# Optimization experiments

Measured on AMD Instinct MI355X. Metric: run time of the kernel, lower is better.

The kernel has to match this reference:

```python
import jax, jax.numpy as jnp
import numpy as np

N_NODES = 100000
N_EDGES = 3200000
NFEAT, H1, H2, NCLASS = 512, 300, 200, 40


def setup_inputs() -> dict:
    key = jax.random.key(0)
    ks = jax.random.split(key, 8)
    x = jax.random.normal(ks[0], (N_NODES, NFEAT), dtype=jnp.float32)
    edge_index = jax.random.randint(ks[1], (2, N_EDGES), 0, N_NODES, dtype=jnp.int32)
    edge_weight = jax.random.uniform(ks[2], (N_EDGES,), dtype=jnp.float32)
    def glorot(k, fi, fo):
        s = 1.0 / np.sqrt(fi)
        return jax.random.uniform(k, (fi, fo), jnp.float32, -s, s)
    w1 = glorot(ks[3], NFEAT, H1)
    w2 = glorot(ks[4], H1, H2)
    w3 = glorot(ks[5], H2, NCLASS)
    return {
        'x': x, 'edge_index': edge_index, 'edge_weight': edge_weight,
        'w1': w1, 'b1': jnp.zeros((H1,), jnp.float32),
        'w2': w2, 'b2': jnp.zeros((H2,), jnp.float32),
        'w3': w3, 'b3': jnp.zeros((NCLASS,), jnp.float32),
    }


def _gcn_layer(h, edge_index, edge_weight, w, b):
    # support = h @ W ; out = A @ support + b  (A given as weighted edge list)
    support = h @ w                                   # [N, out]
    src, dst = edge_index[0], edge_index[1]
    msgs = support[src] * edge_weight[:, None]        # gather + scale, [E, out]
    agg = jax.ops.segment_sum(msgs, dst, num_segments=h.shape[0])
    return agg + b


def reference(x, edge_index, edge_weight, w1, b1, w2, b2, w3, b3):
    h1 = jax.nn.relu(_gcn_layer(x, edge_index, edge_weight, w1, b1))
    h2 = jax.nn.relu(_gcn_layer(h1, edge_index, edge_weight, w2, b2))
    logits = _gcn_layer(h2, edge_index, edge_weight, w3, b3)
    return jax.nn.softmax(logits, axis=1)
```

## Files before the change

kernel.cpp:

```cpp
#include <hip/hip_runtime.h>
#include <hip/hip_bf16.h>
#include <hip/hip_fp16.h>
#include <math.h>

#define NFEAT 512
#define H1 300
#define H2 200
#define NCLASS 40

typedef __attribute__((ext_vector_type(8))) _Float16 half8;
typedef __attribute__((ext_vector_type(4))) float f32x4;
typedef __attribute__((ext_vector_type(2))) unsigned int u32x2;

__device__ __forceinline__ void stage16(const void* gptr, void* ldsptr) {
    __builtin_amdgcn_global_load_lds(
        (const __attribute__((address_space(1))) unsigned int*)gptr,
        (__attribute__((address_space(3))) unsigned int*)ldsptr,
        16, 0, 0);
}

__device__ __forceinline__ unsigned short f2h(float f) {
    return __half_as_ushort(__float2half(f));
}
__device__ __forceinline__ float h2f(unsigned short u) {
    return __half2float(__ushort_as_half(u));
}
__device__ __forceinline__ float2 h2f2(unsigned int u) {
    __half2 h = *reinterpret_cast<__half2*>(&u);
    return __half22float2(h);
}
__device__ __forceinline__ unsigned pack2h(float a, float b) {
    return (unsigned)f2h(a) | ((unsigned)f2h(b) << 16);
}


__global__ __launch_bounds__(256) void count_dst_kernel(const int* __restrict__ dst,
                                                        int* __restrict__ counts, int E) {
    int i = blockIdx.x * blockDim.x + threadIdx.x;
    if (i < E) atomicAdd(&counts[dst[i]], 1);
}

__global__ __launch_bounds__(1024) void scan_kernel(const int* __restrict__ counts,
                                                    int* __restrict__ row_ptr,
                                                    int* __restrict__ nextp, int N) {
    __shared__ int sums[1024];
    const int tid = threadIdx.x;
    const int CH = (N + 1023) >> 10;
    const int b = tid * CH;
    const int e = min(b + CH, N);
    int s = 0;
    for (int i = b; i < e; i++) s += counts[i];
    sums[tid] = s;
    __syncthreads();
    #pragma unroll
    for (int off = 1; off < 1024; off <<= 1) {
        int t = (tid >= off) ? sums[tid - off] : 0;
        __syncthreads();
        sums[tid] += t;
        __syncthreads();
    }
    int run = (tid > 0) ? sums[tid - 1] : 0;
    for (int i = b; i < e; i++) {
        row_ptr[i] = run;
        nextp[i] = run;
        run += counts[i];
    }
    if (tid == 0) row_ptr[N] = sums[1023];
}

__global__ __launch_bounds__(256) void fill_csr_kernel(const int* __restrict__ src,
                                                       const int* __restrict__ dst,
                                                       const float* __restrict__ ew,
                                                       int* __restrict__ next,
                                                       int2* __restrict__ csr_sw, int E) {
    int i = blockIdx.x * blockDim.x + threadIdx.x;
    if (i < E) {
        int d = dst[i];
        int pos = atomicAdd(&next[d], 1);
        csr_sw[pos] = make_int2(src[i], __float_as_int(ew[i]));
    }
}


__global__ __launch_bounds__(256) void convert_x_kernel(const float* __restrict__ x,
                                                        unsigned short* __restrict__ X16,
                                                        int total8) {
    int stride = gridDim.x * 256;
    for (int i = blockIdx.x * 256 + threadIdx.x; i < total8; i += stride) {
        const float* p = x + (size_t)i * 8;
        float4 a = *(const float4*)p;
        float4 b = *(const float4*)(p + 4);
        half8 h;
        h[0] = (_Float16)a.x; h[1] = (_Float16)a.y;
        h[2] = (_Float16)a.z; h[3] = (_Float16)a.w;
        h[4] = (_Float16)b.x; h[5] = (_Float16)b.y;
        h[6] = (_Float16)b.z; h[7] = (_Float16)b.w;
        *(half8*)(X16 + (size_t)i * 8) = h;
    }
}


__global__ __launch_bounds__(256) void split_weights_kernel(
        const float* __restrict__ w1, const float* __restrict__ w2, const float* __restrict__ w3,
        unsigned short* __restrict__ W1H, unsigned short* __restrict__ W1L,
        unsigned short* __restrict__ W2H, unsigned short* __restrict__ W2L,
        unsigned short* __restrict__ W3H, unsigned short* __restrict__ W3L) {
    int i = blockIdx.x * 256 + threadIdx.x;
    const float* w; unsigned short *H, *L; int K, N, KP;
    if (i < 163840) {
        w = w1; H = W1H; L = W1L; K = 512; N = 300; KP = 512;
    } else if (i < 163840 + 81920) {
        i -= 163840; w = w2; H = W2H; L = W2L; K = 300; N = 200; KP = 320;
    } else {
        i -= 245760; w = w3; H = W3H; L = W3L; K = 200; N = 40; KP = 256;
    }
    int n = i / KP, k = i - n * KP;
    float a = (n < N && k < K) ? w[(size_t)k * N + n] : 0.f;
    unsigned short h = f2h(a);
    H[i] = h;
    L[i] = f2h(a - h2f(h));
}


template <int KPAD, int NT, bool AF32>
__global__ __launch_bounds__(256, 3) void gemm_f16_kernel(
        const void* __restrict__ A_,
        const unsigned short* __restrict__ Bhi, const unsigned short* __restrict__ Blo,
        unsigned short* __restrict__ C, int M, int NP, int MT) {
    __shared__ short Bs_hi[4096];
    __shared__ short Bs_lo[4096];

    const int id = blockIdx.x;
    const int g  = id / (8 * NT);
    const int r  = id % (8 * NT);
    const int nt = r >> 3;
    const int x  = r & 7;
    const int mt = g * 8 + x;
    if (mt >= MT) return;

    const int tid = threadIdx.x;
    const int wave = tid >> 6, lane = tid & 63;
    const int lm = lane & 15, quad = lane >> 4;
    const int bm = mt * 256, bn = nt * 64;

    f32x4 acc[4][4] = {};

    for (int k0 = 0; k0 < KPAD; k0 += 64) {
        #pragma unroll
        for (int i = 0; i < 2; i++) {
            int t = i * 256 + tid;
            int n = t >> 3;
            int c = (t & 7) ^ (n & 7);
            size_t goff = (size_t)(bn + n) * KPAD + (size_t)(k0 + c * 8);
            int lbase = (i * 256 + wave * 64) * 8;
            stage16(Bhi + goff, Bs_hi + lbase);
            stage16(Blo + goff, Bs_lo + lbase);
        }
        __syncthreads();

        #pragma unroll
        for (int h = 0; h < 2; h++) {
            const int cidx = h * 4 + quad;
            half8 a[4], bh[4], bl[4];
            #pragma unroll
            for (int i = 0; i < 4; i++) {
                int row = bm + wave * 64 + i * 16 + lm;
                row = row < M ? row : M - 1;
                size_t off = (size_t)row * KPAD + (size_t)(k0 + cidx * 8);
                if (AF32) {
                    const float* ap = (const float*)A_ + off;
                    float4 p = *(const float4*)ap;
                    float4 q = *(const float4*)(ap + 4);
                    half8 t8;
                    t8[0] = (_Float16)p.x; t8[1] = (_Float16)p.y;
                    t8[2] = (_Float16)p.z; t8[3] = (_Float16)p.w;
                    t8[4] = (_Float16)q.x; t8[5] = (_Float16)q.y;
                    t8[6] = (_Float16)q.z; t8[7] = (_Float16)q.w;
                    a[i] = t8;
                } else {
                    a[i] = *(const half8*)((const unsigned short*)A_ + off);
                }
            }
            #pragma unroll
            for (int j = 0; j < 4; j++) {
                int n = j * 16 + lm;
                int off = (n * 8 + (cidx ^ (n & 7))) * 8;
                bh[j] = *(const half8*)(Bs_hi + off);
                bl[j] = *(const half8*)(Bs_lo + off);
            }
            #pragma unroll
            for (int i = 0; i < 4; i++)
                #pragma unroll
                for (int j = 0; j < 4; j++) {
                    acc[i][j] = __builtin_amdgcn_mfma_f32_16x16x32_f16(a[i], bh[j], acc[i][j], 0, 0, 0);
                    acc[i][j] = __builtin_amdgcn_mfma_f32_16x16x32_f16(a[i], bl[j], acc[i][j], 0, 0, 0);
                }
        }
        __syncthreads();
    }

    #pragma unroll
    for (int i = 0; i < 4; i++) {
        #pragma unroll
        for (int j = 0; j < 4; j++) {
            #pragma unroll
            for (int r2 = 0; r2 < 4; r2++) {
                int row = bm + wave * 64 + i * 16 + quad * 4 + r2;
                int col = bn + j * 16 + lm;
                if (row < M)
                    C[(size_t)row * NP + col] = f2h(acc[i][j][r2]);
            }
        }
    }
}


template <bool W> struct GVsel { typedef uint2 T; };
template <> struct GVsel<true> { typedef uint4 T; };

__device__ __forceinline__ void fmaN(float* acc, uint4 g, float w) {
    float2 a;
    a = h2f2(g.x); acc[0] += w * a.x; acc[1] += w * a.y;
    a = h2f2(g.y); acc[2] += w * a.x; acc[3] += w * a.y;
    a = h2f2(g.z); acc[4] += w * a.x; acc[5] += w * a.y;
    a = h2f2(g.w); acc[6] += w * a.x; acc[7] += w * a.y;
}
__device__ __forceinline__ void fmaN(float* acc, uint2 g, float w) {
    float2 a;
    a = h2f2(g.x); acc[0] += w * a.x; acc[1] += w * a.y;
    a = h2f2(g.y); acc[2] += w * a.x; acc[3] += w * a.y;
}

template <int F, int NP>
__global__ __launch_bounds__(256) void spmm_relu_f16_kernel(
        const int* __restrict__ row_ptr, const int2* __restrict__ csr_sw,
        const unsigned short* __restrict__ support, const float* __restrict__ bias,
        unsigned short* __restrict__ outp, int N) {
    constexpr bool WIDE = (NP > 256);
    constexpr int LPE = WIDE ? NP / 8 : NP / 4;
    constexpr int AK  = WIDE ? 8 : 4;
    typedef typename GVsel<WIDE>::T GV;

    const int lane = threadIdx.x & 63;
    const int nwaves = gridDim.x * 4;
    const int lc = WIDE ? min(lane, LPE - 1) : lane;

    for (int row = blockIdx.x * 4 + (threadIdx.x >> 6); row < N; row += nwaves) {
        const int beg = row_ptr[row], end = row_ptr[row + 1];
        const int deg = end - beg;
        float acc[AK];
        #pragma unroll
        for (int k = 0; k < AK; k++) acc[k] = 0.f;

        auto csr_load = [&](int b) -> int2 {
            int idx = min(beg + (b << 2) + min(lane, 3), end - 1);
            return csr_sw[idx];
        };
        auto bcast = [&](int2 cs, int b, int* s, float* w) {
            int base = beg + (b << 2);
            #pragma unroll
            for (int q = 0; q < 4; q++) {
                s[q] = __builtin_amdgcn_readlane(cs.x, q);
                float wv = __uint_as_float((unsigned)__builtin_amdgcn_readlane(cs.y, q));
                w[q] = (base + q < end) ? wv : 0.f;
            }
        };
        auto issue = [&](GV* A, const int* s) {
            #pragma unroll
            for (int q = 0; q < 4; q++) {
                const unsigned short* sp = support + (size_t)s[q] * NP;
                A[q] = *(const GV*)(sp + lc * AK);
            }
        };
        auto consume = [&](const GV* A, const float* w) {
            #pragma unroll
            for (int q = 0; q < 4; q++) fmaN(acc, A[q], w[q]);
        };

        if (deg > 0) {
            const int nb = (deg + 3) >> 2;
            int sa[4]; float wa[4];
            int sb[4]; float wb[4];
            GV A[4], B[4];

            int2 cs = csr_load(0);
            bcast(cs, 0, sa, wa);
            issue(A, sa);
            int b = 0;
            while (b + 1 < nb) {
                int2 cs2 = csr_load(b + 1);
                bcast(cs2, b + 1, sb, wb);
                issue(B, sb);
                consume(A, wa);
                b++;
                if (b + 1 < nb) {
                    cs = csr_load(b + 1);
                    bcast(cs, b + 1, sa, wa);
                    issue(A, sa);
                    consume(B, wb);
                    b++;
                } else {
                    consume(B, wb);
                    b++;
                }
            }
            if (b < nb) consume(A, wa);
        }

        if constexpr (WIDE) {
            if (lane < LPE) {
                half8 o;
                #pragma unroll
                for (int k = 0; k < 8; k++) {
                    int f = lane * 8 + k;
                    float v = (f < F) ? fmaxf(acc[k] + bias[f], 0.f) : 0.f;
                    o[k] = (_Float16)v;
                }
                *(half8*)(outp + (size_t)row * NP + lane * 8) = o;
            }
        } else {
            bool real = lane < F / 4;
            float4 bb = real ? ((const float4*)bias)[lane] : make_float4(0, 0, 0, 0);
            float v0 = real ? fmaxf(acc[0] + bb.x, 0.f) : 0.f;
            float v1 = real ? fmaxf(acc[1] + bb.y, 0.f) : 0.f;
            float v2 = real ? fmaxf(acc[2] + bb.z, 0.f) : 0.f;
            float v3 = real ? fmaxf(acc[3] + bb.w, 0.f) : 0.f;
            u32x2 w;
            w.x = pack2h(v0, v1);
            w.y = pack2h(v2, v3);
            *(u32x2*)(outp + (size_t)row * NP + lane * 4) = w;
        }
    }
}


__global__ __launch_bounds__(256) void spmm_softmax_kernel(
        const int* __restrict__ row_ptr, const int2* __restrict__ csr_sw,
        const unsigned short* __restrict__ support, const float* __restrict__ bias,
        float* __restrict__ out, int N) {
    const int lane = threadIdx.x & 63;
    const int nwaves = gridDim.x * 4;

    const int g = lane / 20;
    const int t = lane - g * 20;
    const bool lact = lane < 60;

    for (int row = blockIdx.x * 4 + (threadIdx.x >> 6); row < N; row += nwaves) {
        int beg = row_ptr[row], end = row_ptr[row + 1];

        float a0 = 0.f, a1 = 0.f;
        for (int e = beg; e < end; e += 3) {
            int ei = e + g;
            bool v = lact && (ei < end);
            int2 sw = csr_sw[v ? ei : beg];
            float w = v ? __int_as_float(sw.y) : 0.f;
            unsigned u = *(const unsigned*)(support + (size_t)sw.x * 64 + t * 2);
            float2 aa = h2f2(u);
            a0 += w * aa.x;
            a1 += w * aa.y;
        }
        a0 += __shfl(a0, lane + 20) + __shfl(a0, lane + 40);
        a1 += __shfl(a1, lane + 20) + __shfl(a1, lane + 40);

        const bool act = lane < 20;
        float v0 = 0.f, v1 = 0.f, m = -INFINITY;
        if (act) {
            float2 bb = ((const float2*)bias)[t];
            v0 = a0 + bb.x;
            v1 = a1 + bb.y;
            m = fmaxf(v0, v1);
        }
        #pragma unroll
        for (int off = 16; off; off >>= 1) m = fmaxf(m, __shfl_xor(m, off));
        float e0 = 0.f, e1 = 0.f;
        if (act) { e0 = expf(v0 - m); e1 = expf(v1 - m); }
        float s = e0 + e1;
        #pragma unroll
        for (int off = 16; off; off >>= 1) s += __shfl_xor(s, off);
        if (act) {
            float inv = 1.f / s;
            *(float2*)(out + (size_t)row * NCLASS + t * 2) = make_float2(e0 * inv, e1 * inv);
        }
    }
}


extern "C" void kernel_launch(void* const* d_in, const int* in_sizes, int n_in,
                              void* d_out, int out_size, void* d_ws, size_t ws_size,
                              hipStream_t stream) {
    const float* x   = (const float*)d_in[0];
    const int*   ei  = (const int*)d_in[1];
    const float* ew  = (const float*)d_in[2];
    const float* w1  = (const float*)d_in[3];
    const float* b1  = (const float*)d_in[4];
    const float* w2  = (const float*)d_in[5];
    const float* b2  = (const float*)d_in[6];
    const float* w3  = (const float*)d_in[7];
    const float* b3  = (const float*)d_in[8];
    float* out = (float*)d_out;

    const int N = in_sizes[0] / NFEAT;
    const int E = in_sizes[2];
    const int* src = ei;
    const int* dst = ei + E;

    const int KP1 = 512, NP1 = 320, NT1 = 5;
    const int KP2 = 320, NP2 = 256, NT2 = 4;
    const int KP3 = 256, NP3 = 64,  NT3 = 1;

    char* base = (char*)d_ws;
    unsigned short* X16 = (unsigned short*)(base);
    unsigned short* H1H = (unsigned short*)(base);
    unsigned short* H2H = (unsigned short*)(base);

    unsigned short* support = (unsigned short*)(base + 102400256);

    size_t wo = 102400256 + 64000256;
    auto walloc = [&](size_t bytes) { void* r = base + wo; wo += (bytes + 255) & ~(size_t)255; return r; };
    unsigned short* W1H = (unsigned short*)walloc((size_t)NP1 * KP1 * 2);
    unsigned short* W1L = (unsigned short*)walloc((size_t)NP1 * KP1 * 2);
    unsigned short* W2H = (unsigned short*)walloc((size_t)NP2 * KP2 * 2);
    unsigned short* W2L = (unsigned short*)walloc((size_t)NP2 * KP2 * 2);
    unsigned short* W3H = (unsigned short*)walloc((size_t)NP3 * KP3 * 2);
    unsigned short* W3L = (unsigned short*)walloc((size_t)NP3 * KP3 * 2);
    int*  counts  = (int*)walloc((size_t)N * 4);
    int*  row_ptr = (int*)walloc((size_t)(N + 1) * 4);
    int*  nextp   = (int*)walloc((size_t)N * 4);
    int2* csr_sw  = (int2*)walloc((size_t)E * 8);

    const int MT = (N + 255) / 256;
    const int G  = (MT + 7) / 8;
    const int SPMM_BLOCKS = 2048;

    hipMemsetAsync(counts, 0, (size_t)N * 4, stream);
    count_dst_kernel<<<(E + 255) / 256, 256, 0, stream>>>(dst, counts, E);
    scan_kernel<<<1, 1024, 0, stream>>>(counts, row_ptr, nextp, N);
    fill_csr_kernel<<<(E + 255) / 256, 256, 0, stream>>>(src, dst, ew, nextp, csr_sw, E);

    split_weights_kernel<<<1024, 256, 0, stream>>>(w1, w2, w3, W1H, W1L, W2H, W2L, W3H, W3L);
    convert_x_kernel<<<2048, 256, 0, stream>>>(x, X16, N * NFEAT / 8);

    gemm_f16_kernel<KP1, NT1, false><<<G * 8 * NT1, 256, 0, stream>>>(
        X16, W1H, W1L, support, N, NP1, MT);
    spmm_relu_f16_kernel<H1, NP1><<<SPMM_BLOCKS, 256, 0, stream>>>(row_ptr, csr_sw, support, b1, H1H, N);

    gemm_f16_kernel<KP2, NT2, false><<<G * 8 * NT2, 256, 0, stream>>>(
        H1H, W2H, W2L, support, N, NP2, MT);
    spmm_relu_f16_kernel<H2, NP2><<<SPMM_BLOCKS, 256, 0, stream>>>(row_ptr, csr_sw, support, b2, H2H, N);

    gemm_f16_kernel<KP3, NT3, false><<<G * 8 * NT3, 256, 0, stream>>>(
        H2H, W3H, W3L, support, N, NP3, MT);
    spmm_softmax_kernel<<<SPMM_BLOCKS, 256, 0, stream>>>(row_ptr, csr_sw, support, b3, out, N);
}
```

Before: 1.725 ms.

## Launch one wave per row and triple-buffer SpMM gathers from single CSR load

The SpMM kernels drop the grid-stride loop and launch one wave per destination row. For rows with at most 64 edges, the relu SpMM loads all edge indices and weights once per lane, broadcasts them with readlane, and keeps three batches of gathers in flight instead of two. Rows above 64 edges fall back to a simple serial loop. The aim is more memory-level parallelism and less per-batch CSR reloading, at the cost of higher register pressure and a slow path for high-degree rows.

```diff
diff --git a/kernel.cpp b/kernel.cpp
--- a/kernel.cpp
+++ b/kernel.cpp
@@ -242,94 +242,97 @@
     typedef typename GVsel<WIDE>::T GV;
 
     const int lane = threadIdx.x & 63;
-    const int nwaves = gridDim.x * 4;
+    const int row = blockIdx.x * 4 + (threadIdx.x >> 6);
+    if (row >= N) return;
     const int lc = WIDE ? min(lane, LPE - 1) : lane;
 
-    for (int row = blockIdx.x * 4 + (threadIdx.x >> 6); row < N; row += nwaves) {
-        const int beg = row_ptr[row], end = row_ptr[row + 1];
-        const int deg = end - beg;
-        float acc[AK];
+    const int beg = row_ptr[row], end = row_ptr[row + 1];
+    const int deg = end - beg;
+
+    float acc[AK];
+    #pragma unroll
+    for (int k = 0; k < AK; k++) acc[k] = 0.f;
+
+    if (deg > 0 && deg <= 64) {
+        const int2 cs = csr_sw[beg + min(lane, deg - 1)];
+        const int sx = cs.x;
+        const int wb = (lane < deg) ? cs.y : 0;
+
+        const int nb = (deg + 3) >> 2;
+
+        GV b0[4], b1[4], b2[4];
+
+        #define ISSUE(B, bq)                                                        \
+            do {                                                                    \
+                _Pragma("unroll")                                                   \
+                for (int q = 0; q < 4; q++) {                                       \
+                    int s = __builtin_amdgcn_readlane(sx, (bq) * 4 + q);            \
+                    const unsigned short* sp = support + (size_t)s * NP;            \
+                    B[q] = *(const GV*)(sp + lc * AK);                              \
+                }                                                                   \
+            } while (0)
+        #define CONSUME(B, bq)                                                      \
+            do {                                                                    \
+                _Pragma("unroll")                                                   \
+                for (int q = 0; q < 4; q++) {                                       \
+                    float w = __uint_as_float(                                      \
+                        (unsigned)__builtin_amdgcn_readlane(wb, (bq) * 4 + q));     \
+                    fmaN(acc, B[q], w);                                             \
+                }                                                                   \
+            } while (0)
+
+        ISSUE(b0, 0);
+        if (nb > 1) ISSUE(b1, 1);
+        if (nb > 2) ISSUE(b2, 2);
         #pragma unroll
-        for (int k = 0; k < AK; k++) acc[k] = 0.f;
-
-        auto csr_load = [&](int b) -> int2 {
-            int idx = min(beg + (b << 2) + min(lane, 3), end - 1);
-            return csr_sw[idx];
-        };
-        auto bcast = [&](int2 cs, int b, int* s, float* w) {
-            int base = beg + (b << 2);
-            #pragma unroll
-            for (int q = 0; q < 4; q++) {
-                s[q] = __builtin_amdgcn_readlane(cs.x, q);
-                float wv = __uint_as_float((unsigned)__builtin_amdgcn_readlane(cs.y, q));
-                w[q] = (base + q < end) ? wv : 0.f;
-            }
-        };
-        auto issue = [&](GV* A, const int* s) {
-            #pragma unroll
-            for (int q = 0; q < 4; q++) {
-                const unsigned short* sp = support + (size_t)s[q] * NP;
-                A[q] = *(const GV*)(sp + lc * AK);
-            }
-        };
-        auto consume = [&](const GV* A, const float* w) {
-            #pragma unroll
-            for (int q = 0; q < 4; q++) fmaN(acc, A[q], w[q]);
-        };
-
-        if (deg > 0) {
-            const int nb = (deg + 3) >> 2;
-            int sa[4]; float wa[4];
-            int sb[4]; float wb[4];
-            GV A[4], B[4];
-
-            int2 cs = csr_load(0);
-            bcast(cs, 0, sa, wa);
-            issue(A, sa);
-            int b = 0;
-            while (b + 1 < nb) {
-                int2 cs2 = csr_load(b + 1);
-                bcast(cs2, b + 1, sb, wb);
-                issue(B, sb);
-                consume(A, wa);
-                b++;
-                if (b + 1 < nb) {
-                    cs = csr_load(b + 1);
-                    bcast(cs, b + 1, sa, wa);
-                    issue(A, sa);
-                    consume(B, wb);
-                    b++;
+        for (int b = 0; b < 16; b++) {
+            if (b < nb) {
+                if ((b % 3) == 0) {
+                    CONSUME(b0, b);
+                    if (b + 3 < nb) ISSUE(b0, b + 3);
+                } else if ((b % 3) == 1) {
+                    CONSUME(b1, b);
+                    if (b + 3 < nb) ISSUE(b1, b + 3);
                 } else {
-                    consume(B, wb);
-                    b++;
+                    CONSUME(b2, b);
+                    if (b + 3 < nb) ISSUE(b2, b + 3);
                 }
             }
-            if (b < nb) consume(A, wa);
-        }
-
-        if constexpr (WIDE) {
-            if (lane < LPE) {
-                half8 o;
-                #pragma unroll
-                for (int k = 0; k < 8; k++) {
-                    int f = lane * 8 + k;
-                    float v = (f < F) ? fmaxf(acc[k] + bias[f], 0.f) : 0.f;
-                    o[k] = (_Float16)v;
-                }
-                *(half8*)(outp + (size_t)row * NP + lane * 8) = o;
+        }
+        #undef ISSUE
+        #undef CONSUME
+    } else if (deg > 64) {
+        for (int e = beg; e < end; e++) {
+            int2 sw = csr_sw[e];
+            float w = __int_as_float(sw.y);
+            const unsigned short* sp = support + (size_t)sw.x * NP;
+            GV g = *(const GV*)(sp + lc * AK);
+            fmaN(acc, g, w);
+        }
+    }
+
+    if constexpr (WIDE) {
+        if (lane < LPE) {
+            half8 o;
+            #pragma unroll
+            for (int k = 0; k < 8; k++) {
+                int f = lane * 8 + k;
+                float v = (f < F) ? fmaxf(acc[k] + bias[f], 0.f) : 0.f;
+                o[k] = (_Float16)v;
             }
-        } else {
-            bool real = lane < F / 4;
-            float4 bb = real ? ((const float4*)bias)[lane] : make_float4(0, 0, 0, 0);
-            float v0 = real ? fmaxf(acc[0] + bb.x, 0.f) : 0.f;
-            float v1 = real ? fmaxf(acc[1] + bb.y, 0.f) : 0.f;
-            float v2 = real ? fmaxf(acc[2] + bb.z, 0.f) : 0.f;
-            float v3 = real ? fmaxf(acc[3] + bb.w, 0.f) : 0.f;
-            u32x2 w;
-            w.x = pack2h(v0, v1);
-            w.y = pack2h(v2, v3);
-            *(u32x2*)(outp + (size_t)row * NP + lane * 4) = w;
-        }
+            *(half8*)(outp + (size_t)row * NP + lane * 8) = o;
+        }
+    } else {
+        bool real = lane < F / 4;
+        float4 bb = real ? ((const float4*)bias)[lane] : make_float4(0, 0, 0, 0);
+        float v0 = real ? fmaxf(acc[0] + bb.x, 0.f) : 0.f;
+        float v1 = real ? fmaxf(acc[1] + bb.y, 0.f) : 0.f;
+        float v2 = real ? fmaxf(acc[2] + bb.z, 0.f) : 0.f;
+        float v3 = real ? fmaxf(acc[3] + bb.w, 0.f) : 0.f;
+        u32x2 w;
+        w.x = pack2h(v0, v1);
+        w.y = pack2h(v2, v3);
+        *(u32x2*)(outp + (size_t)row * NP + lane * 4) = w;
     }
 }
 
@@ -338,49 +341,47 @@
         const int* __restrict__ row_ptr, const int2* __restrict__ csr_sw,
         const unsigned short* __restrict__ support, const float* __restrict__ bias,
         float* __restrict__ out, int N) {
-    const int lane = threadIdx.x & 63;
-    const int nwaves = gridDim.x * 4;
+    int row = blockIdx.x * 4 + (threadIdx.x >> 6);
+    int lane = threadIdx.x & 63;
+    if (row >= N) return;
+    int beg = row_ptr[row], end = row_ptr[row + 1];
 
     const int g = lane / 20;
     const int t = lane - g * 20;
     const bool lact = lane < 60;
 
-    for (int row = blockIdx.x * 4 + (threadIdx.x >> 6); row < N; row += nwaves) {
-        int beg = row_ptr[row], end = row_ptr[row + 1];
-
-        float a0 = 0.f, a1 = 0.f;
-        for (int e = beg; e < end; e += 3) {
-            int ei = e + g;
-            bool v = lact && (ei < end);
-            int2 sw = csr_sw[v ? ei : beg];
-            float w = v ? __int_as_float(sw.y) : 0.f;
-            unsigned u = *(const unsigned*)(support + (size_t)sw.x * 64 + t * 2);
-            float2 aa = h2f2(u);
-            a0 += w * aa.x;
-            a1 += w * aa.y;
-        }
-        a0 += __shfl(a0, lane + 20) + __shfl(a0, lane + 40);
-        a1 += __shfl(a1, lane + 20) + __shfl(a1, lane + 40);
-
-        const bool act = lane < 20;
-        float v0 = 0.f, v1 = 0.f, m = -INFINITY;
-        if (act) {
-            float2 bb = ((const float2*)bias)[t];
-            v0 = a0 + bb.x;
-            v1 = a1 + bb.y;
-            m = fmaxf(v0, v1);
-        }
-        #pragma unroll
-        for (int off = 16; off; off >>= 1) m = fmaxf(m, __shfl_xor(m, off));
-        float e0 = 0.f, e1 = 0.f;
-        if (act) { e0 = expf(v0 - m); e1 = expf(v1 - m); }
-        float s = e0 + e1;
-        #pragma unroll
-        for (int off = 16; off; off >>= 1) s += __shfl_xor(s, off);
-        if (act) {
-            float inv = 1.f / s;
-            *(float2*)(out + (size_t)row * NCLASS + t * 2) = make_float2(e0 * inv, e1 * inv);
-        }
+    float a0 = 0.f, a1 = 0.f;
+    for (int e = beg; e < end; e += 3) {
+        int ei = e + g;
+        bool v = lact && (ei < end);
+        int2 sw = csr_sw[v ? ei : beg];
+        float w = v ? __int_as_float(sw.y) : 0.f;
+        unsigned u = *(const unsigned*)(support + (size_t)sw.x * 64 + t * 2);
+        float2 aa = h2f2(u);
+        a0 += w * aa.x;
+        a1 += w * aa.y;
+    }
+    a0 += __shfl(a0, lane + 20) + __shfl(a0, lane + 40);
+    a1 += __shfl(a1, lane + 20) + __shfl(a1, lane + 40);
+
+    const bool act = lane < 20;
+    float v0 = 0.f, v1 = 0.f, m = -INFINITY;
+    if (act) {
+        float2 bb = ((const float2*)bias)[t];
+        v0 = a0 + bb.x;
+        v1 = a1 + bb.y;
+        m = fmaxf(v0, v1);
+    }
+    #pragma unroll
+    for (int off = 16; off; off >>= 1) m = fmaxf(m, __shfl_xor(m, off));
+    float e0 = 0.f, e1 = 0.f;
+    if (act) { e0 = expf(v0 - m); e1 = expf(v1 - m); }
+    float s = e0 + e1;
+    #pragma unroll
+    for (int off = 16; off; off >>= 1) s += __shfl_xor(s, off);
+    if (act) {
+        float inv = 1.f / s;
+        *(float2*)(out + (size_t)row * NCLASS + t * 2) = make_float2(e0 * inv, e1 * inv);
     }
 }
 
@@ -430,7 +431,7 @@
 
     const int MT = (N + 255) / 256;
     const int G  = (MT + 7) / 8;
-    const int SPMM_BLOCKS = 2048;
+    const int wgs = (N + 3) / 4;
 
     hipMemsetAsync(counts, 0, (size_t)N * 4, stream);
     count_dst_kernel<<<(E + 255) / 256, 256, 0, stream>>>(dst, counts, E);
@@ -442,13 +443,13 @@
 
     gemm_f16_kernel<KP1, NT1, false><<<G * 8 * NT1, 256, 0, stream>>>(
         X16, W1H, W1L, support, N, NP1, MT);
-    spmm_relu_f16_kernel<H1, NP1><<<SPMM_BLOCKS, 256, 0, stream>>>(row_ptr, csr_sw, support, b1, H1H, N);
+    spmm_relu_f16_kernel<H1, NP1><<<wgs, 256, 0, stream>>>(row_ptr, csr_sw, support, b1, H1H, N);
 
     gemm_f16_kernel<KP2, NT2, false><<<G * 8 * NT2, 256, 0, stream>>>(
         H1H, W2H, W2L, support, N, NP2, MT);
-    spmm_relu_f16_kernel<H2, NP2><<<SPMM_BLOCKS, 256, 0, stream>>>(row_ptr, csr_sw, support, b2, H2H, N);
+    spmm_relu_f16_kernel<H2, NP2><<<wgs, 256, 0, stream>>>(row_ptr, csr_sw, support, b2, H2H, N);
 
     gemm_f16_kernel<KP3, NT3, false><<<G * 8 * NT3, 256, 0, stream>>>(
         H2H, W3H, W3L, support, N, NP3, MT);
-    spmm_softmax_kernel<<<SPMM_BLOCKS, 256, 0, stream>>>(row_ptr, csr_sw, support, b3, out, N);
-}
+    spmm_softmax_kernel<<<wgs, 256, 0, stream>>>(row_ptr, csr_sw, support, b3, out, N);
+}
```

Result: no change. 1.708 ms (-1.0%).
